# Kernel optimization log

Measured on AMD Instinct MI355X. Metric: run time of the kernel, lower is better.

Reference implementation:

```python
import jax, jax.numpy as jnp
import numpy as np

NUM_CODES = 512
CODE_DIM = 64
COMMITMENT_COST = 0.25


def setup_inputs() -> dict:
    key = jax.random.key(0)
    k1, k2 = jax.random.split(key)
    latents = jax.random.normal(k1, (32, 64, 64, CODE_DIM), dtype=jnp.float32)
    # torch init: uniform(-1/num_codes, 1/num_codes)
    codebook = jax.random.uniform(
        k2, (NUM_CODES, CODE_DIM), dtype=jnp.float32,
        minval=-1.0 / NUM_CODES, maxval=1.0 / NUM_CODES)
    return {"latents": latents, "codebook": codebook}


def reference(latents, codebook):
    shape = latents.shape
    flat = latents.reshape(-1, CODE_DIM)  # [N, D]
    # argmin of squared distance == argmin of cdist(p=2) distance.
    x2 = jnp.sum(flat * flat, axis=-1, keepdims=True)           # [N, 1]
    c2 = jnp.sum(codebook * codebook, axis=-1)                   # [K]
    d2 = x2 - 2.0 * (flat @ codebook.T) + c2[None, :]            # [N, K]
    codes_flat = jnp.argmin(d2, axis=-1)                         # [N] int
    codes = codes_flat.reshape(shape[:-1])

    quantized = codebook[codes_flat].reshape(shape)              # gather

    commitment = jnp.mean(jnp.square(latents - jax.lax.stop_gradient(quantized)))
    codebook_loss = jnp.mean(jnp.square(quantized - jax.lax.stop_gradient(latents)))

    # straight-through estimator
    quantized_st = latents + jax.lax.stop_gradient(quantized - latents)

    # perplexity histogram
    counts = jnp.bincount(codes_flat, length=NUM_CODES).astype(jnp.float32)
    probs = counts / jnp.sum(counts)
    entropy = -jnp.sum(probs * jnp.log(probs + 1e-10))
    perplexity = jnp.exp(entropy)

    return (quantized_st, codes,
            commitment * COMMITMENT_COST, codebook_loss, perplexity)
```

## Files before the change

### kernel.cpp

```cpp
#include <hip/hip_runtime.h>
#include <math.h>

#define N_ROWS 131072
#define DIMS 64
#define K_CODES 512
#define XS_STRIDE 68

typedef __attribute__((ext_vector_type(8))) short bf16x8;
typedef __attribute__((ext_vector_type(4))) float f32x4;

union B8 { uint4 u; bf16x8 h; };

__device__ inline unsigned bpack(float a, float b) {
  unsigned ua = __float_as_uint(a), ub = __float_as_uint(b);
  ua = (ua + 0x7FFFu + ((ua >> 16) & 1u)) >> 16;
  ub = (ub + 0x7FFFu + ((ub >> 16) & 1u)) >> 16;
  return ua | (ub << 16);
}

__device__ inline float exact_dot(const float* __restrict__ xr, const float* __restrict__ cr) {
  float m = 0.f;
  #pragma unroll
  for (int d4 = 0; d4 < 16; ++d4) {
    const float4 c = *(const float4*)&cr[d4 * 4];
    const float4 x = *(const float4*)&xr[d4 * 4];
    m = fmaf(x.x, c.x, m);
    m = fmaf(x.y, c.y, m);
    m = fmaf(x.z, c.z, m);
    m = fmaf(x.w, c.w, m);
  }
  return m;
}

__global__ __launch_bounds__(256) void vq_init(const float* __restrict__ codebook,
                                               int* __restrict__ bins,
                                               float* __restrict__ c2g,
                                               float* __restrict__ cmax2p,
                                               uint4* __restrict__ cbB) {
  #pragma clang fp contract(off)
  __shared__ float smax[256];
  const int t = threadIdx.x;
  const int b = blockIdx.x;
  if (b == 0) {
    for (int k = t; k < K_CODES; k += 256) bins[k] = 0;
    float lmax = 0.f;
    for (int k = t; k < K_CODES; k += 256) {
      const float* cr = codebook + k * DIMS;
      float r[8];
      #pragma unroll
      for (int j = 0; j < 8; ++j) r[j] = cr[j] * cr[j];
      for (int i = 8; i < 64; i += 8) {
        #pragma unroll
        for (int j = 0; j < 8; ++j) r[j] += cr[i + j] * cr[i + j];
      }
      const float c2 = ((r[0] + r[1]) + (r[2] + r[3])) + ((r[4] + r[5]) + (r[6] + r[7]));
      c2g[k] = c2;
      lmax = fmaxf(lmax, c2);
    }
    smax[t] = lmax;
    __syncthreads();
    for (int s = 128; s > 0; s >>= 1) {
      if (t < s) smax[t] = fmaxf(smax[t], smax[t + s]);
      __syncthreads();
    }
    if (t == 0) *cmax2p = smax[0];
  }
  if (b < 16) {
    const int e = b * 256 + t;
    const int ct = e >> 7;
    const int q = e & 127;
    const int lane_id = q >> 1;
    const int half = q & 1;
    const int code = ct * 16 + (lane_id & 15);
    const int dbase = ((lane_id >> 4) * 8) + half * 32;
    const float* src = codebook + code * DIMS + dbase;
    const float4 a = *(const float4*)&src[0];
    const float4 c = *(const float4*)&src[4];
    uint4 u;
    u.x = bpack(a.x, a.y);
    u.y = bpack(a.z, a.w);
    u.z = bpack(c.x, c.y);
    u.w = bpack(c.z, c.w);
    cbB[e] = u;
  }
}

__global__ __launch_bounds__(256, 4) void vq_main(const float* __restrict__ latents,
                                                  const float* __restrict__ codebook,
                                                  const uint4* __restrict__ cbB,
                                                  const float* __restrict__ c2g,
                                                  const float* __restrict__ cmax2p,
                                                  float* __restrict__ out_st,
                                                  float* __restrict__ out_codes,
                                                  int* __restrict__ bins,
                                                  double* __restrict__ loss_part) {
  #pragma clang fp contract(off)
  __shared__ __align__(16) float xs[64 * XS_STRIDE];
  __shared__ float x2s[64];
  __shared__ float c2s[K_CODES];
  __shared__ float thr[64];
  __shared__ float pmin[4][64];
  __shared__ int cand_cnt[64];
  __shared__ int cand_k[64][16];
  __shared__ int rowk[64];
  __shared__ float pvv[4][64];
  __shared__ int pkk[4][64];
  __shared__ int ovf_rows[64];
  __shared__ int ovf_cnt;
  __shared__ double wsum[4];

  const int t = threadIdx.x;
  const int lane = t & 63;
  const int w = t >> 6;
  const int m = lane & 15;
  const int kq = lane >> 4;
  const int row0 = blockIdx.x * 64;

  {
    const float4* src = (const float4*)(latents + (size_t)row0 * DIMS);
    #pragma unroll
    for (int p = 0; p < 4; ++p) {
      const int f = p * 256 + t;
      *(float4*)&xs[(f >> 4) * XS_STRIDE + (f & 15) * 4] = src[f];
    }
    c2s[t] = c2g[t];
    c2s[t + 256] = c2g[t + 256];
    if (t < 64) cand_cnt[t] = 0;
    if (t == 0) ovf_cnt = 0;
  }
  __syncthreads();

  if (t < 64) {
    const float* xr = xs + t * XS_STRIDE;
    float r[8];
    #pragma unroll
    for (int j = 0; j < 8; ++j) r[j] = xr[j] * xr[j];
    #pragma unroll
    for (int i = 8; i < 64; i += 8) {
      #pragma unroll
      for (int j = 0; j < 8; ++j) r[j] += xr[i + j] * xr[i + j];
    }
    x2s[t] = ((r[0] + r[1]) + (r[2] + r[3])) + ((r[4] + r[5]) + (r[6] + r[7]));
  }
  __syncthreads();

  bf16x8 af0[4], af1[4];
  #pragma unroll
  for (int T = 0; T < 4; ++T) {
    const float* xr = xs + (T * 16 + m) * XS_STRIDE + kq * 8;
    const float4 a0 = *(const float4*)&xr[0];
    const float4 a1 = *(const float4*)&xr[4];
    const float4 b0 = *(const float4*)&xr[32];
    const float4 b1 = *(const float4*)&xr[36];
    B8 pa, pb;
    pa.u.x = bpack(a0.x, a0.y); pa.u.y = bpack(a0.z, a0.w);
    pa.u.z = bpack(a1.x, a1.y); pa.u.w = bpack(a1.z, a1.w);
    pb.u.x = bpack(b0.x, b0.y); pb.u.y = bpack(b0.z, b0.w);
    pb.u.z = bpack(b1.x, b1.y); pb.u.w = bpack(b1.z, b1.w);
    af0[T] = pa.h;
    af1[T] = pb.h;
  }

  float x2r[4][4];
  #pragma unroll
  for (int T = 0; T < 4; ++T)
    #pragma unroll
    for (int j = 0; j < 4; ++j) x2r[T][j] = x2s[T * 16 + kq * 4 + j];
  const float cmax = sqrtf(*cmax2p) * 1.0001f;
  const int ct0 = w * 8;

  float mv[4][4];
  #pragma unroll
  for (int T = 0; T < 4; ++T)
    #pragma unroll
    for (int j = 0; j < 4; ++j) mv[T][j] = __builtin_inff();

  B8 cb0, cb1, nb0, nb1;
  cb0.u = cbB[ct0 * 128 + lane * 2 + 0];
  cb1.u = cbB[ct0 * 128 + lane * 2 + 1];
  #pragma unroll 1
  for (int q = 0; q < 8; ++q) {
    const int ct = ct0 + q;
    if (q < 7) {
      nb0.u = cbB[(ct + 1) * 128 + lane * 2 + 0];
      nb1.u = cbB[(ct + 1) * 128 + lane * 2 + 1];
    }
    const float c2v = c2s[ct * 16 + m];
    #pragma unroll
    for (int T = 0; T < 4; ++T) {
      f32x4 acc = {0.f, 0.f, 0.f, 0.f};
      acc = __builtin_amdgcn_mfma_f32_16x16x32_bf16(af0[T], cb0.h, acc, 0, 0, 0);
      acc = __builtin_amdgcn_mfma_f32_16x16x32_bf16(af1[T], cb1.h, acc, 0, 0, 0);
      #pragma unroll
      for (int j = 0; j < 4; ++j) {
        const float s = (x2r[T][j] - 2.0f * acc[j]) + c2v;
        mv[T][j] = fminf(mv[T][j], s);
      }
    }
    cb0 = nb0;
    cb1 = nb1;
  }
  #pragma unroll
  for (int T = 0; T < 4; ++T)
    #pragma unroll
    for (int j = 0; j < 4; ++j) {
      float v = mv[T][j];
      #pragma unroll
      for (int off = 1; off < 16; off <<= 1) v = fminf(v, __shfl_xor(v, off));
      mv[T][j] = v;
    }
  if (m == 0) {
    #pragma unroll
    for (int T = 0; T < 4; ++T)
      #pragma unroll
      for (int j = 0; j < 4; ++j) pmin[w][T * 16 + kq * 4 + j] = mv[T][j];
  }
  __syncthreads();
  if (t < 64) {
    const float gmin = fminf(fminf(pmin[0][t], pmin[1][t]), fminf(pmin[2][t], pmin[3][t]));
    thr[t] = gmin + (sqrtf(x2s[t]) * cmax * 0.0427f + 1e-3f);
  }
  __syncthreads();

  float thrr[4][4];
  #pragma unroll
  for (int T = 0; T < 4; ++T)
    #pragma unroll
    for (int j = 0; j < 4; ++j) thrr[T][j] = thr[T * 16 + kq * 4 + j];

  cb0.u = cbB[ct0 * 128 + lane * 2 + 0];
  cb1.u = cbB[ct0 * 128 + lane * 2 + 1];
  #pragma unroll 1
  for (int q = 0; q < 8; ++q) {
    const int ct = ct0 + q;
    if (q < 7) {
      nb0.u = cbB[(ct + 1) * 128 + lane * 2 + 0];
      nb1.u = cbB[(ct + 1) * 128 + lane * 2 + 1];
    }
    const float c2v = c2s[ct * 16 + m];
    const int k = ct * 16 + m;
    #pragma unroll
    for (int T = 0; T < 4; ++T) {
      f32x4 acc = {0.f, 0.f, 0.f, 0.f};
      acc = __builtin_amdgcn_mfma_f32_16x16x32_bf16(af0[T], cb0.h, acc, 0, 0, 0);
      acc = __builtin_amdgcn_mfma_f32_16x16x32_bf16(af1[T], cb1.h, acc, 0, 0, 0);
      #pragma unroll
      for (int j = 0; j < 4; ++j) {
        const float s = (x2r[T][j] - 2.0f * acc[j]) + c2v;
        if (s <= thrr[T][j]) {
          const int rr = T * 16 + kq * 4 + j;
          const int pos = atomicAdd(&cand_cnt[rr], 1);
          if (pos < 16) cand_k[rr][pos] = k;
        }
      }
    }
    cb0 = nb0;
    cb1 = nb1;
  }
  __syncthreads();

  {
    const int rr = t & 63;
    const int ph = t >> 6;
    const int cnt = cand_cnt[rr];
    float bv = __builtin_inff();
    int bk = 0x7fffffff;
    if (cnt <= 16) {
      const float* xr = xs + rr * XS_STRIDE;
      const float x2e = x2s[rr];
      for (int c = ph; c < cnt; c += 4) {
        const int k = cand_k[rr][c];
        const float M = exact_dot(xr, codebook + k * DIMS);
        const float s = (x2e - 2.0f * M) + c2s[k];
        if (s < bv || (s == bv && k < bk)) { bv = s; bk = k; }
      }
    } else if (ph == 0) {
      const int p = atomicAdd(&ovf_cnt, 1);
      ovf_rows[p] = rr;
    }
    pvv[ph][rr] = bv;
    pkk[ph][rr] = bk;
  }
  __syncthreads();
  if (t < 64) {
    float bv = pvv[0][t];
    int bk = pkk[0][t];
    #pragma unroll
    for (int ph = 1; ph < 4; ++ph) {
      const float v = pvv[ph][t];
      const int k = pkk[ph][t];
      if (v < bv || (v == bv && k < bk)) { bv = v; bk = k; }
    }
    rowk[t] = bk;
  }
  __syncthreads();

  if (w == 0) {
    const int no = ovf_cnt;
    for (int o = 0; o < no; ++o) {
      const int rr = ovf_rows[o];
      const float* xr = xs + rr * XS_STRIDE;
      const float x2e = x2s[rr];
      float bv = __builtin_inff();
      int bk = 0x7fffffff;
      for (int k = lane; k < K_CODES; k += 64) {
        const float M = exact_dot(xr, codebook + k * DIMS);
        const float s = (x2e - 2.0f * M) + c2s[k];
        if (s < bv || (s == bv && k < bk)) { bv = s; bk = k; }
      }
      #pragma unroll
      for (int off = 1; off < 64; off <<= 1) {
        const float ov = __shfl_xor(bv, off);
        const int oi = __shfl_xor(bk, off);
        if (ov < bv || (ov == bv && oi < bk)) { bv = ov; bk = oi; }
      }
      if (lane == 0) rowk[rr] = bk;
    }
  }
  __syncthreads();

  if (t < 64) {
    const int k = rowk[t];
    out_codes[row0 + t] = (float)k;
    atomicAdd(&bins[k], 1);
  }
  double dacc = 0.0;
  {
    float4* dst = (float4*)out_st + (size_t)row0 * 16;
    #pragma unroll
    for (int p = 0; p < 4; ++p) {
      const int f = p * 256 + t;
      const int r = f >> 4;
      const int d4 = f & 15;
      const int k = rowk[r];
      const float4 q = *(const float4*)&codebook[k * DIMS + d4 * 4];
      const float4 l = *(const float4*)&xs[r * XS_STRIDE + d4 * 4];
      float4 o;
      o.x = l.x + (q.x - l.x);
      o.y = l.y + (q.y - l.y);
      o.z = l.z + (q.z - l.z);
      o.w = l.w + (q.w - l.w);
      dst[f] = o;
      const float dx = l.x - q.x, dy = l.y - q.y, dz = l.z - q.z, dw = l.w - q.w;
      dacc += (double)dx * (double)dx;
      dacc += (double)dy * (double)dy;
      dacc += (double)dz * (double)dz;
      dacc += (double)dw * (double)dw;
    }
  }
  #pragma unroll
  for (int off = 32; off > 0; off >>= 1) dacc += __shfl_down(dacc, off);
  if (lane == 0) wsum[w] = dacc;
  __syncthreads();
  if (t == 0) loss_part[blockIdx.x] = (wsum[0] + wsum[1]) + (wsum[2] + wsum[3]);
}

__global__ __launch_bounds__(512) void vq_finalize(const int* __restrict__ bins,
                                                   const double* __restrict__ loss_part,
                                                   float* __restrict__ out3) {
  __shared__ double red[512];
  __shared__ double redl[512];
  const int t = threadIdx.x;
  const double p = (double)bins[t] / 131072.0;
  red[t] = -p * log(p + 1e-10);
  redl[t] = (loss_part[t] + loss_part[t + 512]) + (loss_part[t + 1024] + loss_part[t + 1536]);
  __syncthreads();
  for (int s = 256; s > 0; s >>= 1) {
    if (t < s) { red[t] += red[t + s]; redl[t] += redl[t + s]; }
    __syncthreads();
  }
  if (t == 0) {
    const double mean = redl[0] / 8388608.0;
    out3[0] = (float)(0.25 * mean);
    out3[1] = (float)mean;
    out3[2] = (float)exp(red[0]);
  }
}

extern "C" void kernel_launch(void* const* d_in, const int* in_sizes, int n_in,
                              void* d_out, int out_size, void* d_ws, size_t ws_size,
                              hipStream_t stream) {
  const float* latents = (const float*)d_in[0];
  const float* codebook = (const float*)d_in[1];

  float* out = (float*)d_out;
  float* out_st = out;
  float* out_codes = out + (size_t)N_ROWS * DIMS;
  float* out3 = out_codes + N_ROWS;

  char* ws = (char*)d_ws;
  double* loss_part = (double*)ws;
  int* bins = (int*)(ws + 16384);
  float* c2g = (float*)(ws + 18432);
  float* cmax2 = (float*)(ws + 20480);
  uint4* cbB = (uint4*)(ws + 21504);

  hipLaunchKernelGGL(vq_init, dim3(16), dim3(256), 0, stream,
                     codebook, bins, c2g, cmax2, cbB);
  hipLaunchKernelGGL(vq_main, dim3(2048), dim3(256), 0, stream,
                     latents, codebook, cbB, c2g, cmax2, out_st, out_codes, bins, loss_part);
  hipLaunchKernelGGL(vq_finalize, dim3(1), dim3(512), 0, stream,
                     bins, loss_part, out3);
}
```

Measured before the change: 152.6 us.

## Fold -2 scale and c2 into MFMA, parallelize init and norm computation

```diff
diff --git a/kernel.cpp b/kernel.cpp
--- a/kernel.cpp
+++ b/kernel.cpp
@@ -35,38 +35,12 @@
 __global__ __launch_bounds__(256) void vq_init(const float* __restrict__ codebook,
                                                int* __restrict__ bins,
                                                float* __restrict__ c2g,
-                                               float* __restrict__ cmax2p,
                                                uint4* __restrict__ cbB) {
   #pragma clang fp contract(off)
-  __shared__ float smax[256];
   const int t = threadIdx.x;
   const int b = blockIdx.x;
-  if (b == 0) {
-    for (int k = t; k < K_CODES; k += 256) bins[k] = 0;
-    float lmax = 0.f;
-    for (int k = t; k < K_CODES; k += 256) {
-      const float* cr = codebook + k * DIMS;
-      float r[8];
-      #pragma unroll
-      for (int j = 0; j < 8; ++j) r[j] = cr[j] * cr[j];
-      for (int i = 8; i < 64; i += 8) {
-        #pragma unroll
-        for (int j = 0; j < 8; ++j) r[j] += cr[i + j] * cr[i + j];
-      }
-      const float c2 = ((r[0] + r[1]) + (r[2] + r[3])) + ((r[4] + r[5]) + (r[6] + r[7]));
-      c2g[k] = c2;
-      lmax = fmaxf(lmax, c2);
-    }
-    smax[t] = lmax;
-    __syncthreads();
-    for (int s = 128; s > 0; s >>= 1) {
-      if (t < s) smax[t] = fmaxf(smax[t], smax[t + s]);
-      __syncthreads();
-    }
-    if (t == 0) *cmax2p = smax[0];
-  }
-  if (b < 16) {
-    const int e = b * 256 + t;
+  if (t < 64) {
+    const int e = b * 64 + t;
     const int ct = e >> 7;
     const int q = e & 127;
     const int lane_id = q >> 1;
@@ -77,11 +51,24 @@
     const float4 a = *(const float4*)&src[0];
     const float4 c = *(const float4*)&src[4];
     uint4 u;
-    u.x = bpack(a.x, a.y);
-    u.y = bpack(a.z, a.w);
-    u.z = bpack(c.x, c.y);
-    u.w = bpack(c.z, c.w);
+    u.x = bpack(-2.f * a.x, -2.f * a.y);
+    u.y = bpack(-2.f * a.z, -2.f * a.w);
+    u.z = bpack(-2.f * c.x, -2.f * c.y);
+    u.w = bpack(-2.f * c.z, -2.f * c.w);
     cbB[e] = u;
+  } else if (t < 72) {
+    const int k = b * 8 + (t - 64);
+    const float* cr = codebook + k * DIMS;
+    float r[8];
+    #pragma unroll
+    for (int j = 0; j < 8; ++j) r[j] = cr[j] * cr[j];
+    for (int i = 8; i < 64; i += 8) {
+      #pragma unroll
+      for (int j = 0; j < 8; ++j) r[j] += cr[i + j] * cr[i + j];
+    }
+    c2g[k] = ((r[0] + r[1]) + (r[2] + r[3])) + ((r[4] + r[5]) + (r[6] + r[7]));
+  } else if (t < 80) {
+    bins[b * 8 + (t - 72)] = 0;
   }
 }
 
@@ -89,15 +76,16 @@
                                                   const float* __restrict__ codebook,
                                                   const uint4* __restrict__ cbB,
                                                   const float* __restrict__ c2g,
-                                                  const float* __restrict__ cmax2p,
                                                   float* __restrict__ out_st,
                                                   float* __restrict__ out_codes,
                                                   int* __restrict__ bins,
                                                   double* __restrict__ loss_part) {
   #pragma clang fp contract(off)
   __shared__ __align__(16) float xs[64 * XS_STRIDE];
+  __shared__ float x2p[64][4];
   __shared__ float x2s[64];
   __shared__ float c2s[K_CODES];
+  __shared__ float wmaxs[4];
   __shared__ float thr[64];
   __shared__ float pmin[4][64];
   __shared__ int cand_cnt[64];
@@ -130,19 +118,27 @@
   }
   __syncthreads();
 
-  if (t < 64) {
-    const float* xr = xs + t * XS_STRIDE;
-    float r[8];
-    #pragma unroll
-    for (int j = 0; j < 8; ++j) r[j] = xr[j] * xr[j];
-    #pragma unroll
-    for (int i = 8; i < 64; i += 8) {
-      #pragma unroll
-      for (int j = 0; j < 8; ++j) r[j] += xr[i + j] * xr[i + j];
-    }
-    x2s[t] = ((r[0] + r[1]) + (r[2] + r[3])) + ((r[4] + r[5]) + (r[6] + r[7]));
-  }
-  __syncthreads();
+  {
+    const int rr = t >> 2, ph = t & 3;
+    const float* xr = xs + rr * XS_STRIDE;
+    float2 v = *(const float2*)&xr[2 * ph];
+    float ra = v.x * v.x, rb = v.y * v.y;
+    #pragma unroll
+    for (int i8 = 1; i8 < 8; ++i8) {
+      v = *(const float2*)&xr[i8 * 8 + 2 * ph];
+      ra += v.x * v.x;
+      rb += v.y * v.y;
+    }
+    x2p[rr][ph] = ra + rb;
+  }
+  {
+    float mm = fmaxf(c2s[t], c2s[t + 256]);
+    #pragma unroll
+    for (int off = 1; off < 64; off <<= 1) mm = fmaxf(mm, __shfl_xor(mm, off));
+    if (lane == 0) wmaxs[w] = mm;
+  }
+  __syncthreads();
+  if (t < 64) x2s[t] = (x2p[t][0] + x2p[t][1]) + (x2p[t][2] + x2p[t][3]);
 
   bf16x8 af0[4], af1[4];
   #pragma unroll
@@ -161,12 +157,6 @@
     af1[T] = pb.h;
   }
 
-  float x2r[4][4];
-  #pragma unroll
-  for (int T = 0; T < 4; ++T)
-    #pragma unroll
-    for (int j = 0; j < 4; ++j) x2r[T][j] = x2s[T * 16 + kq * 4 + j];
-  const float cmax = sqrtf(*cmax2p) * 1.0001f;
   const int ct0 = w * 8;
 
   float mv[4][4];
@@ -175,30 +165,50 @@
     #pragma unroll
     for (int j = 0; j < 4; ++j) mv[T][j] = __builtin_inff();
 
-  B8 cb0, cb1, nb0, nb1;
-  cb0.u = cbB[ct0 * 128 + lane * 2 + 0];
-  cb1.u = cbB[ct0 * 128 + lane * 2 + 1];
-  #pragma unroll 1
-  for (int q = 0; q < 8; ++q) {
-    const int ct = ct0 + q;
-    if (q < 7) {
-      nb0.u = cbB[(ct + 1) * 128 + lane * 2 + 0];
-      nb1.u = cbB[(ct + 1) * 128 + lane * 2 + 1];
-    }
-    const float c2v = c2s[ct * 16 + m];
-    #pragma unroll
-    for (int T = 0; T < 4; ++T) {
-      f32x4 acc = {0.f, 0.f, 0.f, 0.f};
-      acc = __builtin_amdgcn_mfma_f32_16x16x32_bf16(af0[T], cb0.h, acc, 0, 0, 0);
-      acc = __builtin_amdgcn_mfma_f32_16x16x32_bf16(af1[T], cb1.h, acc, 0, 0, 0);
-      #pragma unroll
-      for (int j = 0; j < 4; ++j) {
-        const float s = (x2r[T][j] - 2.0f * acc[j]) + c2v;
-        mv[T][j] = fminf(mv[T][j], s);
-      }
-    }
-    cb0 = nb0;
-    cb1 = nb1;
+  {
+    B8 sa0, sb0, sa1, sb1;
+    sa0.u = cbB[(ct0 + 0) * 128 + lane * 2 + 0];
+    sb0.u = cbB[(ct0 + 0) * 128 + lane * 2 + 1];
+    sa1.u = cbB[(ct0 + 1) * 128 + lane * 2 + 0];
+    sb1.u = cbB[(ct0 + 1) * 128 + lane * 2 + 1];
+    #pragma unroll 1
+    for (int qq = 0; qq < 4; ++qq) {
+      const int ct = ct0 + qq * 2;
+      {
+        B8 na, nb;
+        if (qq < 3) {
+          na.u = cbB[(ct + 2) * 128 + lane * 2 + 0];
+          nb.u = cbB[(ct + 2) * 128 + lane * 2 + 1];
+        }
+        const float c2v = c2s[ct * 16 + m];
+        #pragma unroll
+        for (int T = 0; T < 4; ++T) {
+          f32x4 acc = {c2v, c2v, c2v, c2v};
+          acc = __builtin_amdgcn_mfma_f32_16x16x32_bf16(af0[T], sa0.h, acc, 0, 0, 0);
+          acc = __builtin_amdgcn_mfma_f32_16x16x32_bf16(af1[T], sb0.h, acc, 0, 0, 0);
+          #pragma unroll
+          for (int j = 0; j < 4; ++j) mv[T][j] = fminf(mv[T][j], acc[j]);
+        }
+        if (qq < 3) { sa0 = na; sb0 = nb; }
+      }
+      {
+        B8 na, nb;
+        if (qq < 3) {
+          na.u = cbB[(ct + 3) * 128 + lane * 2 + 0];
+          nb.u = cbB[(ct + 3) * 128 + lane * 2 + 1];
+        }
+        const float c2v = c2s[(ct + 1) * 16 + m];
+        #pragma unroll
+        for (int T = 0; T < 4; ++T) {
+          f32x4 acc = {c2v, c2v, c2v, c2v};
+          acc = __builtin_amdgcn_mfma_f32_16x16x32_bf16(af0[T], sa1.h, acc, 0, 0, 0);
+          acc = __builtin_amdgcn_mfma_f32_16x16x32_bf16(af1[T], sb1.h, acc, 0, 0, 0);
+          #pragma unroll
+          for (int j = 0; j < 4; ++j) mv[T][j] = fminf(mv[T][j], acc[j]);
+        }
+        if (qq < 3) { sa1 = na; sb1 = nb; }
+      }
+    }
   }
   #pragma unroll
   for (int T = 0; T < 4; ++T)
@@ -218,44 +228,75 @@
   __syncthreads();
   if (t < 64) {
     const float gmin = fminf(fminf(pmin[0][t], pmin[1][t]), fminf(pmin[2][t], pmin[3][t]));
-    thr[t] = gmin + (sqrtf(x2s[t]) * cmax * 0.0427f + 1e-3f);
-  }
-  __syncthreads();
-
-  float thrr[4][4];
-  #pragma unroll
-  for (int T = 0; T < 4; ++T)
-    #pragma unroll
-    for (int j = 0; j < 4; ++j) thrr[T][j] = thr[T * 16 + kq * 4 + j];
-
-  cb0.u = cbB[ct0 * 128 + lane * 2 + 0];
-  cb1.u = cbB[ct0 * 128 + lane * 2 + 1];
-  #pragma unroll 1
-  for (int q = 0; q < 8; ++q) {
-    const int ct = ct0 + q;
-    if (q < 7) {
-      nb0.u = cbB[(ct + 1) * 128 + lane * 2 + 0];
-      nb1.u = cbB[(ct + 1) * 128 + lane * 2 + 1];
-    }
-    const float c2v = c2s[ct * 16 + m];
-    const int k = ct * 16 + m;
-    #pragma unroll
-    for (int T = 0; T < 4; ++T) {
-      f32x4 acc = {0.f, 0.f, 0.f, 0.f};
-      acc = __builtin_amdgcn_mfma_f32_16x16x32_bf16(af0[T], cb0.h, acc, 0, 0, 0);
-      acc = __builtin_amdgcn_mfma_f32_16x16x32_bf16(af1[T], cb1.h, acc, 0, 0, 0);
+    const float cmax2 = fmaxf(fmaxf(wmaxs[0], wmaxs[1]), fmaxf(wmaxs[2], wmaxs[3]));
+    thr[t] = gmin + (sqrtf(x2s[t]) * sqrtf(cmax2) * 0.0157f + 1e-3f);
+  }
+  __syncthreads();
+
+  {
+    float thrr[4][4];
+    #pragma unroll
+    for (int T = 0; T < 4; ++T)
       #pragma unroll
-      for (int j = 0; j < 4; ++j) {
-        const float s = (x2r[T][j] - 2.0f * acc[j]) + c2v;
-        if (s <= thrr[T][j]) {
-          const int rr = T * 16 + kq * 4 + j;
-          const int pos = atomicAdd(&cand_cnt[rr], 1);
-          if (pos < 16) cand_k[rr][pos] = k;
-        }
-      }
-    }
-    cb0 = nb0;
-    cb1 = nb1;
+      for (int j = 0; j < 4; ++j) thrr[T][j] = thr[T * 16 + kq * 4 + j];
+
+    B8 sa0, sb0, sa1, sb1;
+    sa0.u = cbB[(ct0 + 0) * 128 + lane * 2 + 0];
+    sb0.u = cbB[(ct0 + 0) * 128 + lane * 2 + 1];
+    sa1.u = cbB[(ct0 + 1) * 128 + lane * 2 + 0];
+    sb1.u = cbB[(ct0 + 1) * 128 + lane * 2 + 1];
+    #pragma unroll 1
+    for (int qq = 0; qq < 4; ++qq) {
+      const int ct = ct0 + qq * 2;
+      {
+        B8 na, nb;
+        if (qq < 3) {
+          na.u = cbB[(ct + 2) * 128 + lane * 2 + 0];
+          nb.u = cbB[(ct + 2) * 128 + lane * 2 + 1];
+        }
+        const float c2v = c2s[ct * 16 + m];
+        const int k = ct * 16 + m;
+        #pragma unroll
+        for (int T = 0; T < 4; ++T) {
+          f32x4 acc = {c2v, c2v, c2v, c2v};
+          acc = __builtin_amdgcn_mfma_f32_16x16x32_bf16(af0[T], sa0.h, acc, 0, 0, 0);
+          acc = __builtin_amdgcn_mfma_f32_16x16x32_bf16(af1[T], sb0.h, acc, 0, 0, 0);
+          #pragma unroll
+          for (int j = 0; j < 4; ++j) {
+            if (acc[j] <= thrr[T][j]) {
+              const int rr = T * 16 + kq * 4 + j;
+              const int pos = atomicAdd(&cand_cnt[rr], 1);
+              if (pos < 16) cand_k[rr][pos] = k;
+            }
+          }
+        }
+        if (qq < 3) { sa0 = na; sb0 = nb; }
+      }
+      {
+        B8 na, nb;
+        if (qq < 3) {
+          na.u = cbB[(ct + 3) * 128 + lane * 2 + 0];
+          nb.u = cbB[(ct + 3) * 128 + lane * 2 + 1];
+        }
+        const float c2v = c2s[(ct + 1) * 16 + m];
+        const int k = (ct + 1) * 16 + m;
+        #pragma unroll
+        for (int T = 0; T < 4; ++T) {
+          f32x4 acc = {c2v, c2v, c2v, c2v};
+          acc = __builtin_amdgcn_mfma_f32_16x16x32_bf16(af0[T], sa1.h, acc, 0, 0, 0);
+          acc = __builtin_amdgcn_mfma_f32_16x16x32_bf16(af1[T], sb1.h, acc, 0, 0, 0);
+          #pragma unroll
+          for (int j = 0; j < 4; ++j) {
+            if (acc[j] <= thrr[T][j]) {
+              const int rr = T * 16 + kq * 4 + j;
+              const int pos = atomicAdd(&cand_cnt[rr], 1);
+              if (pos < 16) cand_k[rr][pos] = k;
+            }
+          }
+        }
+        if (qq < 3) { sa1 = na; sb1 = nb; }
+      }
+    }
   }
   __syncthreads();
 
@@ -392,13 +433,12 @@
   double* loss_part = (double*)ws;
   int* bins = (int*)(ws + 16384);
   float* c2g = (float*)(ws + 18432);
-  float* cmax2 = (float*)(ws + 20480);
   uint4* cbB = (uint4*)(ws + 21504);
 
-  hipLaunchKernelGGL(vq_init, dim3(16), dim3(256), 0, stream,
-                     codebook, bins, c2g, cmax2, cbB);
+  hipLaunchKernelGGL(vq_init, dim3(64), dim3(256), 0, stream,
+                     codebook, bins, c2g, cbB);
   hipLaunchKernelGGL(vq_main, dim3(2048), dim3(256), 0, stream,
-                     latents, codebook, cbB, c2g, cmax2, out_st, out_codes, bins, loss_part);
+                     latents, codebook, cbB, c2g, out_st, out_codes, bins, loss_part);
   hipLaunchKernelGGL(vq_finalize, dim3(1), dim3(512), 0, stream,
                      bins, loss_part, out3);
 }
```

After: 140.6 us. 7.9% less time.

## Fuse finalize into main kernel via last-block ticket and parallelize init

Applied to the files above, without the earlier changes.

```diff
diff --git a/kernel.cpp b/kernel.cpp
--- a/kernel.cpp
+++ b/kernel.cpp
@@ -5,6 +5,7 @@
 #define DIMS 64
 #define K_CODES 512
 #define XS_STRIDE 68
+#define NBLK 2048
 
 typedef __attribute__((ext_vector_type(8))) short bf16x8;
 typedef __attribute__((ext_vector_type(4))) float f32x4;
@@ -35,38 +36,13 @@
 __global__ __launch_bounds__(256) void vq_init(const float* __restrict__ codebook,
                                                int* __restrict__ bins,
                                                float* __restrict__ c2g,
-                                               float* __restrict__ cmax2p,
-                                               uint4* __restrict__ cbB) {
+                                               uint4* __restrict__ cbB,
+                                               int* __restrict__ done_cnt) {
   #pragma clang fp contract(off)
-  __shared__ float smax[256];
   const int t = threadIdx.x;
   const int b = blockIdx.x;
-  if (b == 0) {
-    for (int k = t; k < K_CODES; k += 256) bins[k] = 0;
-    float lmax = 0.f;
-    for (int k = t; k < K_CODES; k += 256) {
-      const float* cr = codebook + k * DIMS;
-      float r[8];
-      #pragma unroll
-      for (int j = 0; j < 8; ++j) r[j] = cr[j] * cr[j];
-      for (int i = 8; i < 64; i += 8) {
-        #pragma unroll
-        for (int j = 0; j < 8; ++j) r[j] += cr[i + j] * cr[i + j];
-      }
-      const float c2 = ((r[0] + r[1]) + (r[2] + r[3])) + ((r[4] + r[5]) + (r[6] + r[7]));
-      c2g[k] = c2;
-      lmax = fmaxf(lmax, c2);
-    }
-    smax[t] = lmax;
-    __syncthreads();
-    for (int s = 128; s > 0; s >>= 1) {
-      if (t < s) smax[t] = fmaxf(smax[t], smax[t + s]);
-      __syncthreads();
-    }
-    if (t == 0) *cmax2p = smax[0];
-  }
-  if (b < 16) {
-    const int e = b * 256 + t;
+  if (t < 64) {
+    const int e = b * 64 + t;
     const int ct = e >> 7;
     const int q = e & 127;
     const int lane_id = q >> 1;
@@ -82,6 +58,21 @@
     u.z = bpack(c.x, c.y);
     u.w = bpack(c.z, c.w);
     cbB[e] = u;
+  } else if (t < 72) {
+    const int k = b * 8 + (t - 64);
+    const float* cr = codebook + k * DIMS;
+    float r[8];
+    #pragma unroll
+    for (int j = 0; j < 8; ++j) r[j] = cr[j] * cr[j];
+    for (int i = 8; i < 64; i += 8) {
+      #pragma unroll
+      for (int j = 0; j < 8; ++j) r[j] += cr[i + j] * cr[i + j];
+    }
+    c2g[k] = ((r[0] + r[1]) + (r[2] + r[3])) + ((r[4] + r[5]) + (r[6] + r[7]));
+  } else if (t < 80) {
+    bins[b * 8 + (t - 72)] = 0;
+  } else if (t == 80 && b == 0) {
+    *done_cnt = 0;
   }
 }
 
@@ -89,15 +80,17 @@
                                                   const float* __restrict__ codebook,
                                                   const uint4* __restrict__ cbB,
                                                   const float* __restrict__ c2g,
-                                                  const float* __restrict__ cmax2p,
                                                   float* __restrict__ out_st,
                                                   float* __restrict__ out_codes,
                                                   int* __restrict__ bins,
-                                                  double* __restrict__ loss_part) {
+                                                  double* __restrict__ loss_part,
+                                                  int* __restrict__ done_cnt,
+                                                  float* __restrict__ out3) {
   #pragma clang fp contract(off)
   __shared__ __align__(16) float xs[64 * XS_STRIDE];
   __shared__ float x2s[64];
   __shared__ float c2s[K_CODES];
+  __shared__ float wmaxs[4];
   __shared__ float thr[64];
   __shared__ float pmin[4][64];
   __shared__ int cand_cnt[64];
@@ -108,6 +101,7 @@
   __shared__ int ovf_rows[64];
   __shared__ int ovf_cnt;
   __shared__ double wsum[4];
+  __shared__ int ticket_s;
 
   const int t = threadIdx.x;
   const int lane = t & 63;
@@ -141,6 +135,12 @@
       for (int j = 0; j < 8; ++j) r[j] += xr[i + j] * xr[i + j];
     }
     x2s[t] = ((r[0] + r[1]) + (r[2] + r[3])) + ((r[4] + r[5]) + (r[6] + r[7]));
+  }
+  {
+    float mm = fmaxf(c2s[t], c2s[t + 256]);
+    #pragma unroll
+    for (int off = 1; off < 64; off <<= 1) mm = fmaxf(mm, __shfl_xor(mm, off));
+    if (lane == 0) wmaxs[w] = mm;
   }
   __syncthreads();
 
@@ -166,7 +166,6 @@
   for (int T = 0; T < 4; ++T)
     #pragma unroll
     for (int j = 0; j < 4; ++j) x2r[T][j] = x2s[T * 16 + kq * 4 + j];
-  const float cmax = sqrtf(*cmax2p) * 1.0001f;
   const int ct0 = w * 8;
 
   float mv[4][4];
@@ -218,6 +217,7 @@
   __syncthreads();
   if (t < 64) {
     const float gmin = fminf(fminf(pmin[0][t], pmin[1][t]), fminf(pmin[2][t], pmin[3][t]));
+    const float cmax = sqrtf(fmaxf(fmaxf(wmaxs[0], wmaxs[1]), fmaxf(wmaxs[2], wmaxs[3]))) * 1.0001f;
     thr[t] = gmin + (sqrtf(x2s[t]) * cmax * 0.0427f + 1e-3f);
   }
   __syncthreads();
@@ -352,28 +352,38 @@
   for (int off = 32; off > 0; off >>= 1) dacc += __shfl_down(dacc, off);
   if (lane == 0) wsum[w] = dacc;
   __syncthreads();
-  if (t == 0) loss_part[blockIdx.x] = (wsum[0] + wsum[1]) + (wsum[2] + wsum[3]);
-}
-
-__global__ __launch_bounds__(512) void vq_finalize(const int* __restrict__ bins,
-                                                   const double* __restrict__ loss_part,
-                                                   float* __restrict__ out3) {
-  __shared__ double red[512];
-  __shared__ double redl[512];
-  const int t = threadIdx.x;
-  const double p = (double)bins[t] / 131072.0;
-  red[t] = -p * log(p + 1e-10);
-  redl[t] = (loss_part[t] + loss_part[t + 512]) + (loss_part[t + 1024] + loss_part[t + 1536]);
-  __syncthreads();
-  for (int s = 256; s > 0; s >>= 1) {
-    if (t < s) { red[t] += red[t + s]; redl[t] += redl[t + s]; }
+
+  if (t == 0) {
+    loss_part[blockIdx.x] = (wsum[0] + wsum[1]) + (wsum[2] + wsum[3]);
+    __threadfence();
+    ticket_s = atomicAdd(done_cnt, 1);
+  }
+  __syncthreads();
+  if (ticket_s == NBLK - 1) {
+    __threadfence();
+    double* red2 = (double*)xs;
+    double* redl2 = (double*)&xs[512];
+    const int b0 = __hip_atomic_load(&bins[t], __ATOMIC_RELAXED, __HIP_MEMORY_SCOPE_AGENT);
+    const int b1 = __hip_atomic_load(&bins[t + 256], __ATOMIC_RELAXED, __HIP_MEMORY_SCOPE_AGENT);
+    const double p0 = (double)b0 / 131072.0;
+    const double p1 = (double)b1 / 131072.0;
+    red2[t] = (-p0 * log(p0 + 1e-10)) + (-p1 * log(p1 + 1e-10));
+    double lp[8];
+    #pragma unroll
+    for (int i = 0; i < 8; ++i)
+      lp[i] = __hip_atomic_load(&loss_part[t + 256 * i], __ATOMIC_RELAXED, __HIP_MEMORY_SCOPE_AGENT);
+    redl2[t] = ((lp[0] + lp[2]) + (lp[4] + lp[6])) + ((lp[1] + lp[3]) + (lp[5] + lp[7]));
     __syncthreads();
-  }
-  if (t == 0) {
-    const double mean = redl[0] / 8388608.0;
-    out3[0] = (float)(0.25 * mean);
-    out3[1] = (float)mean;
-    out3[2] = (float)exp(red[0]);
+    for (int s = 128; s > 0; s >>= 1) {
+      if (t < s) { red2[t] += red2[t + s]; redl2[t] += redl2[t + s]; }
+      __syncthreads();
+    }
+    if (t == 0) {
+      const double mean = redl2[0] / 8388608.0;
+      out3[0] = (float)(0.25 * mean);
+      out3[1] = (float)mean;
+      out3[2] = (float)exp(red2[0]);
+    }
   }
 }
 
@@ -392,13 +402,12 @@
   double* loss_part = (double*)ws;
   int* bins = (int*)(ws + 16384);
   float* c2g = (float*)(ws + 18432);
-  float* cmax2 = (float*)(ws + 20480);
+  int* done_cnt = (int*)(ws + 20480);
   uint4* cbB = (uint4*)(ws + 21504);
 
-  hipLaunchKernelGGL(vq_init, dim3(16), dim3(256), 0, stream,
-                     codebook, bins, c2g, cmax2, cbB);
-  hipLaunchKernelGGL(vq_main, dim3(2048), dim3(256), 0, stream,
-                     latents, codebook, cbB, c2g, cmax2, out_st, out_codes, bins, loss_part);
-  hipLaunchKernelGGL(vq_finalize, dim3(1), dim3(512), 0, stream,
-                     bins, loss_part, out3);
+  hipLaunchKernelGGL(vq_init, dim3(64), dim3(256), 0, stream,
+                     codebook, bins, c2g, cbB, done_cnt);
+  hipLaunchKernelGGL(vq_main, dim3(NBLK), dim3(256), 0, stream,
+                     latents, codebook, cbB, c2g, out_st, out_codes, bins, loss_part,
+                     done_cnt, out3);
 }
```

Result: slower. 194.2 us (+27.3%).
